# Kernel tuning notes

Measured on AMD Instinct MI355X. Metric: run time of the kernel, lower is better.

## Reference

```python
import jax, jax.numpy as jnp
import numpy as np

B, S, H = 2, 1024, 2048          # batch, seq, hidden
NH, HD = 32, 64                  # heads, head_dim
E, M, K = 8, 1024, 2             # experts, moe_dim, top_k
EPS = 1e-5
ROPE_THETA = 10000.0


def setup_inputs() -> dict:
    key = jax.random.key(0)
    ks = jax.random.split(key, 12)
    sc = lambda *sh: 0.02
    return {
        "hidden_states": jax.random.normal(ks[0], (B, S, H), jnp.float32),
        "w_attn_norm": jnp.ones((H,), jnp.float32),
        "Wq": jax.random.normal(ks[1], (H, H), jnp.float32) * 0.02,
        "Wk": jax.random.normal(ks[2], (H, H), jnp.float32) * 0.02,
        "Wv": jax.random.normal(ks[3], (H, H), jnp.float32) * 0.02,
        "Wo": jax.random.normal(ks[4], (H, H), jnp.float32) * 0.02,
        "w_moe_norm": jnp.ones((H,), jnp.float32),
        "Wr": jax.random.normal(ks[5], (H, E), jnp.float32) * 0.02,
        "Wgate": jax.random.normal(ks[6], (E, H, M), jnp.float32) * 0.02,
        "Wup": jax.random.normal(ks[7], (E, H, M), jnp.float32) * 0.02,
        "Wdown": jax.random.normal(ks[8], (E, M, H), jnp.float32) * 0.02,
    }


def _rmsnorm(x, w):
    return x * jax.lax.rsqrt(jnp.mean(x * x, axis=-1, keepdims=True) + EPS) * w


def _rope_cos_sin(seq_len, dtype):
    inv_freq = 1.0 / (ROPE_THETA ** (jnp.arange(0, HD, 2, dtype=jnp.float32) / HD))
    ang = jnp.arange(seq_len, dtype=jnp.float32)[:, None] * inv_freq[None, :]  # [S, HD/2]
    cos = jnp.concatenate([jnp.cos(ang), jnp.cos(ang)], axis=-1).astype(dtype)  # [S, HD]
    sin = jnp.concatenate([jnp.sin(ang), jnp.sin(ang)], axis=-1).astype(dtype)
    return cos, sin


def _rotate_half(x):
    x1, x2 = jnp.split(x, 2, axis=-1)
    return jnp.concatenate([-x2, x1], axis=-1)


def _attention(x, Wq, Wk, Wv, Wo, mask):
    b, s, _ = x.shape
    def heads(t):  # [b,s,H] -> [b,NH,s,HD]
        return t.reshape(b, s, NH, HD).transpose(0, 2, 1, 3)
    q, k, v = heads(x @ Wq), heads(x @ Wk), heads(x @ Wv)
    cos, sin = _rope_cos_sin(s, x.dtype)
    q = q * cos + _rotate_half(q) * sin
    k = k * cos + _rotate_half(k) * sin
    scores = jnp.einsum("bhqd,bhkd->bhqk", q, k) / jnp.sqrt(jnp.asarray(HD, x.dtype))
    scores = scores + mask  # [1,1,s,s] causal
    attn = jax.nn.softmax(scores, axis=-1)
    out = jnp.einsum("bhqk,bhkd->bhqd", attn, v)
    out = out.transpose(0, 2, 1, 3).reshape(b, s, H)
    return out @ Wo


def _moe(x, Wr, Wgate, Wup, Wdown):
    b, s, _ = x.shape
    xf = x.reshape(b * s, H)  # [T, H]
    logits = xf @ Wr  # [T, E]
    probs = jax.nn.softmax(logits, axis=-1)
    topv, topi = jax.lax.top_k(probs, K)  # [T, K]
    topv = topv / jnp.sum(topv, axis=-1, keepdims=True)
    # combine weights [T, E], zero for unselected experts
    cw = jnp.sum(jax.nn.one_hot(topi, E, dtype=xf.dtype) * topv[..., None], axis=1)
    g = jnp.einsum("th,ehm->etm", xf, Wgate)
    u = jnp.einsum("th,ehm->etm", xf, Wup)
    h = jax.nn.silu(g) * u
    expert_out = jnp.einsum("etm,emh->eth", h, Wdown)  # [E, T, H]
    out = jnp.einsum("eth,te->th", expert_out, cw)
    return out.reshape(b, s, H)


def reference(hidden_states, w_attn_norm, Wq, Wk, Wv, Wo, w_moe_norm, Wr, Wgate, Wup, Wdown):
    b, s, _ = hidden_states.shape
    causal = jnp.triu(jnp.full((s, s), -jnp.inf, hidden_states.dtype), k=1)[None, None]
    residual = hidden_states
    x = _rmsnorm(hidden_states, w_attn_norm)
    x = _attention(x, Wq, Wk, Wv, Wo, causal)
    x = x + residual
    residual = x
    y = _rmsnorm(x, w_moe_norm)
    y = _moe(y, Wr, Wgate, Wup, Wdown)
    return y + residual
```

## Files before the change

kernel.cpp:

```cpp
#include <hip/hip_runtime.h>
#include <hip/hip_bf16.h>
#include <cstdint>

typedef unsigned short u16;
typedef __bf16 bf16x4_t __attribute__((ext_vector_type(4)));
typedef __bf16 bf16x8_t __attribute__((ext_vector_type(8)));
typedef float f32x4_t __attribute__((ext_vector_type(4)));
typedef unsigned short us4_t __attribute__((ext_vector_type(4)));
typedef unsigned short us8_t __attribute__((ext_vector_type(8)));

#define BATCH 2
#define SEQ 1024
#define HID 2048
#define NHEAD 32
#define NEXP 8
#define MDIM 1024
#define T_TOK (BATCH*SEQ)


__device__ __forceinline__ void gload16(const void* g, void* l){
  __builtin_amdgcn_global_load_lds((__attribute__((address_space(1))) void*)(uintptr_t)g,
                                   (__attribute__((address_space(3))) void*)l, 16, 0, 0);
}

__device__ __forceinline__ bf16x8_t ldfrag(const u16* lo){
  bf16x4_t a = *(const bf16x4_t*)lo;
  bf16x4_t b = *(const bf16x4_t*)(lo + 16);
  return __builtin_shufflevector(a, b, 0,1,2,3,4,5,6,7);
}

__device__ __forceinline__ bf16x8_t ldfsw128(const u16* base, int row, int colbyte){
  const char* p = (const char*)base + row*128;
  int sw = (row & 7) << 4;
  bf16x4_t a = *(const bf16x4_t*)(p + (colbyte ^ sw));
  bf16x4_t b = *(const bf16x4_t*)(p + ((colbyte + 32) ^ sw));
  return __builtin_shufflevector(a, b, 0,1,2,3,4,5,6,7);
}

__device__ __forceinline__ bf16x8_t ldfsw64(const u16* base, int row, int colbyte){
  const char* p = (const char*)base + row*64;
  int sw = (row & 3) << 4;
  bf16x4_t a = *(const bf16x4_t*)(p + (colbyte ^ sw));
  bf16x4_t b = *(const bf16x4_t*)(p + ((colbyte + 32) ^ sw));
  return __builtin_shufflevector(a, b, 0,1,2,3,4,5,6,7);
}

__device__ __forceinline__ f32x4_t mfma16(bf16x8_t a, bf16x8_t b, f32x4_t c){
  return __builtin_amdgcn_mfma_f32_16x16x32_bf16(a, b, c, 0, 0, 0);
}

__device__ __forceinline__ u16 f2b(float f){
  __hip_bfloat16 h = __float2bfloat16(f);
  return __builtin_bit_cast(u16, h);
}
__device__ __forceinline__ float b2f(u16 b){
  return __builtin_bit_cast(float, (unsigned int)b << 16);
}
__device__ __forceinline__ void split3v(float v, u16& b1, u16& b2, u16& b3){
  b1 = f2b(v); float f1 = b2f(b1);
  float r1 = v - f1;
  b2 = f2b(r1); float f2 = b2f(b2);
  b3 = f2b(r1 - f2);
}



__global__ __launch_bounds__(256)
void convT(const float* __restrict__ in, u16* __restrict__ out, int R, int C)
{
  __shared__ float t[64][65];
  int bz = blockIdx.z;
  const float* ip = in + (size_t)bz * R * C;
  u16* op = out + (size_t)bz * R * C;
  int r0 = blockIdx.y*64, c0 = blockIdx.x*64;
  int tid = threadIdx.x;
  int lr = tid >> 4;
  int lc = (tid & 15) * 4;
  #pragma unroll
  for (int i = 0; i < 4; i++){
    int r = lr + i*16;
    float4 v = *(const float4*)&ip[(size_t)(r0 + r) * C + c0 + lc];
    t[r][lc] = v.x; t[r][lc+1] = v.y; t[r][lc+2] = v.z; t[r][lc+3] = v.w;
  }
  __syncthreads();
  #pragma unroll
  for (int i = 0; i < 4; i++){
    int c = lr + i*16;
    us4_t o;
    o.x = f2b(t[lc+0][c]); o.y = f2b(t[lc+1][c]);
    o.z = f2b(t[lc+2][c]); o.w = f2b(t[lc+3][c]);
    *(us4_t*)&op[(size_t)(c0 + c) * R + r0 + lc] = o;
  }
}


__global__ __launch_bounds__(256)
void convT3(const float* __restrict__ in, u16* __restrict__ o1, u16* __restrict__ o2,
            u16* __restrict__ o3)
{
  __shared__ float t[64][65];
  int r0 = blockIdx.y*64, c0 = blockIdx.x*64;
  int tid = threadIdx.x;
  int lr = tid >> 4;
  int lc = (tid & 15) * 4;
  #pragma unroll
  for (int i = 0; i < 4; i++){
    int r = lr + i*16;
    float4 v = *(const float4*)&in[(size_t)(r0 + r) * HID + c0 + lc];
    t[r][lc] = v.x; t[r][lc+1] = v.y; t[r][lc+2] = v.z; t[r][lc+3] = v.w;
  }
  __syncthreads();
  if (tid < 128){
    int n  = tid & 63;
    int kb2 = tid >> 6;
    int gn = c0 + n;
    int nb = gn >> 7, sub = (gn >> 4) & 7, fr = gn & 15;
    int kb = (r0 >> 5) + kb2;
    size_t fo = (((size_t)(nb*64 + kb)*8 + sub)*64 + fr*4) * 8;
    #pragma unroll
    for (int fg = 0; fg < 4; fg++){
      us8_t w1, w2, w3;
      #pragma unroll
      for (int j = 0; j < 4; j++){
        u16 b1, b2, b3;
        split3v(t[kb2*32 + fg*4 + j][n], b1, b2, b3);
        w1[j] = b1; w2[j] = b2; w3[j] = b3;
        split3v(t[kb2*32 + fg*4 + 16 + j][n], b1, b2, b3);
        w1[j+4] = b1; w2[j+4] = b2; w3[j+4] = b3;
      }
      *(us8_t*)&o1[fo + fg*8] = w1;
      *(us8_t*)&o2[fo + fg*8] = w2;
      *(us8_t*)&o3[fo + fg*8] = w3;
    }
  }
}


__global__ __launch_bounds__(256)
void rmsnorm3_k(const float* __restrict__ x, const float* __restrict__ w,
                u16* __restrict__ o1, u16* __restrict__ o2, u16* __restrict__ o3)
{
  int row = blockIdx.x;
  const float* xr = x + (size_t)row * HID;
  int tid = threadIdx.x;
  int kb = tid >> 2, fg = tid & 3;
  int kbase = kb*32 + fg*4;
  float4 a = *(const float4*)(xr + kbase);
  float4 b = *(const float4*)(xr + kbase + 16);
  float ss = a.x*a.x + a.y*a.y + a.z*a.z + a.w*a.w
           + b.x*b.x + b.y*b.y + b.z*b.z + b.w*b.w;
  #pragma unroll
  for (int off = 32; off; off >>= 1) ss += __shfl_down(ss, off);
  __shared__ float red[4];
  if ((tid & 63) == 0) red[tid >> 6] = ss;
  __syncthreads();
  float tot = red[0] + red[1] + red[2] + red[3];
  float rs = (float)(1.0 / sqrt((double)tot * (1.0/2048.0) + 1e-5));
  float4 wa = *(const float4*)(w + kbase);
  float4 wb = *(const float4*)(w + kbase + 16);
  float o[8];
  o[0]=a.x*rs*wa.x; o[1]=a.y*rs*wa.y; o[2]=a.z*rs*wa.z; o[3]=a.w*rs*wa.w;
  o[4]=b.x*rs*wb.x; o[5]=b.y*rs*wb.y; o[6]=b.z*rs*wb.z; o[7]=b.w*rs*wb.w;
  us8_t w1, w2, w3;
  #pragma unroll
  for (int j = 0; j < 8; j++){
    u16 b1, b2, b3; split3v(o[j], b1, b2, b3);
    w1[j] = b1; w2[j] = b2; w3[j] = b3;
  }
  int rb = row >> 7, sub = (row >> 4) & 7, fr = row & 15;
  size_t fo = (((size_t)(rb*64 + kb)*8 + sub)*64 + fr*4 + fg) * 8;
  *(us8_t*)&o1[fo] = w1; *(us8_t*)&o2[fo] = w2; *(us8_t*)&o3[fo] = w3;
}


__global__ __launch_bounds__(256)
void rmsnorm_k(const float* __restrict__ x, const float* __restrict__ w,
               u16* __restrict__ ob, float* __restrict__ of, float* __restrict__ oi)
{
  int row = blockIdx.x;
  const float* xr = x + (size_t)row * HID;
  int base = threadIdx.x * 8;
  float4 a = *(const float4*)(xr + base);
  float4 b = *(const float4*)(xr + base + 4);
  float ss = a.x*a.x + a.y*a.y + a.z*a.z + a.w*a.w
           + b.x*b.x + b.y*b.y + b.z*b.z + b.w*b.w;
  #pragma unroll
  for (int off = 32; off; off >>= 1) ss += __shfl_down(ss, off);
  __shared__ float red[4];
  if ((threadIdx.x & 63) == 0) red[threadIdx.x >> 6] = ss;
  __syncthreads();
  float tot = red[0] + red[1] + red[2] + red[3];
  float rs = (float)(1.0 / sqrt((double)tot * (1.0/2048.0) + 1e-5));
  float4 wa = *(const float4*)(w + base);
  float4 wb = *(const float4*)(w + base + 4);
  float o[8];
  o[0]=a.x*rs*wa.x; o[1]=a.y*rs*wa.y; o[2]=a.z*rs*wa.z; o[3]=a.w*rs*wa.w;
  o[4]=b.x*rs*wb.x; o[5]=b.y*rs*wb.y; o[6]=b.z*rs*wb.z; o[7]=b.w*rs*wb.w;
  us4_t p0, p1;
  p0.x=f2b(o[0]); p0.y=f2b(o[1]); p0.z=f2b(o[2]); p0.w=f2b(o[3]);
  p1.x=f2b(o[4]); p1.y=f2b(o[5]); p1.z=f2b(o[6]); p1.w=f2b(o[7]);
  *(us4_t*)&ob[(size_t)row*HID + base] = p0;
  *(us4_t*)&ob[(size_t)row*HID + base + 4] = p1;
  float* orow = of + (size_t)row*HID + base;
  *(float4*)orow = make_float4(o[0],o[1],o[2],o[3]);
  *(float4*)(orow+4) = make_float4(o[4],o[5],o[6],o[7]);
  float* irow = oi + (size_t)row*HID + base;
  *(float4*)irow = a;
  *(float4*)(irow+4) = b;
}


__global__ void rope_table_k(float* ct, float* st){
  int i = blockIdx.x*256 + threadIdx.x;
  int s = i >> 5, j = i & 31;
  double invf = exp(-(double)j / 32.0 * log(10000.0));
  double ang = (double)s * invf;
  ct[i] = (float)cos(ang);
  st[i] = (float)sin(ang);
}


__global__ __launch_bounds__(256, 2)
void gemm_qkv(const u16* __restrict__ A1, const u16* __restrict__ A2, const u16* __restrict__ A3,
              const u16* __restrict__ Wq1, const u16* __restrict__ Wq2, const u16* __restrict__ Wq3,
              const u16* __restrict__ Wk1, const u16* __restrict__ Wk2, const u16* __restrict__ Wk3,
              const u16* __restrict__ Wv1, const u16* __restrict__ Wv2, const u16* __restrict__ Wv3,
              u16* __restrict__ oq1, u16* __restrict__ oq2, u16* __restrict__ oq3,
              u16* __restrict__ ok1, u16* __restrict__ ok2, u16* __restrict__ ok3,
              float* __restrict__ vf,
              const float* __restrict__ ct, const float* __restrict__ st)
{
  __shared__ u16 As[3][128*32];
  __shared__ u16 Bs[3][128*32];
  const int flat = blockIdx.x + 16*blockIdx.y + 256*blockIdx.z;
  const int logical = (flat & 7) * 96 + (flat >> 3);
  const int z  = logical >> 8;
  const int bm = ((logical >> 4) & 15) * 128;
  const int bn = (logical & 15) * 128;
  const int tid = threadIdx.x;
  const int lane = tid & 63;
  const int wave = tid >> 6;
  const int wr = wave >> 1, wc = wave & 1;
  const int fr = lane & 15, fg = lane >> 4;

  f32x4_t acc[4][4] = {};

  const u16* Ap[3] = {A1, A2, A3};
  const u16* Bp[3];
  if (z == 0)      { Bp[0] = Wq1; Bp[1] = Wq2; Bp[2] = Wq3; }
  else if (z == 1) { Bp[0] = Wk1; Bp[1] = Wk2; Bp[2] = Wk3; }
  else             { Bp[0] = Wv1; Bp[1] = Wv2; Bp[2] = Wv3; }
  const u16* gA[3]; const u16* gB[3];
  #pragma unroll
  for (int t = 0; t < 3; t++){
    gA[t] = Ap[t] + (size_t)(bm >> 7) * 64 * 4096 + tid*8;
    gB[t] = Bp[t] + (size_t)(bn >> 7) * 64 * 4096 + tid*8;
  }

  for (int kb = 0; kb < 64; kb++){
    const size_t o = (size_t)kb * 4096;
    #pragma unroll
    for (int t = 0; t < 3; t++){
      gload16(gA[t] + o,        &As[t][tid*8]);
      gload16(gA[t] + o + 2048, &As[t][2048 + tid*8]);
      gload16(gB[t] + o,        &Bs[t][tid*8]);
      gload16(gB[t] + o + 2048, &Bs[t][2048 + tid*8]);
    }
    __syncthreads();
    bf16x8_t bfv[3][4];
    #pragma unroll
    for (int t = 0; t < 3; t++)
      #pragma unroll
      for (int ni = 0; ni < 4; ni++)
        bfv[t][ni] = *(const bf16x8_t*)&Bs[t][(((wc*4 + ni)*64) + fr*4 + fg)*8];
    #pragma unroll
    for (int mi = 0; mi < 4; mi++){
      const int ao = (((wr*4 + mi)*64) + fr*4 + fg)*8;
      bf16x8_t a1 = *(const bf16x8_t*)&As[0][ao];
      bf16x8_t a2 = *(const bf16x8_t*)&As[1][ao];
      bf16x8_t a3 = *(const bf16x8_t*)&As[2][ao];
      #pragma unroll
      for (int ni = 0; ni < 4; ni++){
        f32x4_t c = acc[mi][ni];
        c = mfma16(a3, bfv[0][ni], c);
        c = mfma16(a2, bfv[1][ni], c);
        c = mfma16(a1, bfv[2][ni], c);
        c = mfma16(a2, bfv[0][ni], c);
        c = mfma16(a1, bfv[1][ni], c);
        c = mfma16(a1, bfv[0][ni], c);
        acc[mi][ni] = c;
      }
    }
    __syncthreads();
  }

  if (z < 2){
    u16* O1 = z ? ok1 : oq1;
    u16* O2 = z ? ok2 : oq2;
    u16* O3 = z ? ok3 : oq3;
    #pragma unroll
    for (int mi = 0; mi < 4; mi++)
      #pragma unroll
      for (int r = 0; r < 4; r++){
        int row = bm + wr*64 + mi*16 + fg*4 + r;
        int s = row & (SEQ-1);
        #pragma unroll
        for (int ni = 0; ni < 2; ni++){
          int dlo = ni*16 + fr;
          float c  = ct[s*32 + dlo];
          float sn = st[s*32 + dlo];
          float xl = acc[mi][ni][r], xh = acc[mi][ni+2][r];
          float ol = xl*c - xh*sn;
          float oh = xh*c + xl*sn;
          size_t idx = (size_t)row * HID + bn + wc*64 + ni*16 + fr;
          u16 b1, b2, b3;
          split3v(ol, b1, b2, b3); O1[idx] = b1;    O2[idx] = b2;    O3[idx] = b3;
          split3v(oh, b1, b2, b3); O1[idx+32] = b1; O2[idx+32] = b2; O3[idx+32] = b3;
        }
      }
  } else {
    #pragma unroll
    for (int mi = 0; mi < 4; mi++)
      #pragma unroll
      for (int ni = 0; ni < 4; ni++)
        #pragma unroll
        for (int r = 0; r < 4; r++){
          int row = bm + wr*64 + mi*16 + fg*4 + r;
          int col = bn + wc*64 + ni*16 + fr;
          vf[(size_t)row * HID + col] = acc[mi][ni][r];
        }
  }
}


__global__ __launch_bounds__(256, 2)
void gemm_o(const u16* __restrict__ A1, const u16* __restrict__ A2, const u16* __restrict__ A3,
            const u16* __restrict__ B1, const u16* __restrict__ B2, const u16* __restrict__ B3,
            float* __restrict__ Cf, const float* __restrict__ Res)
{
  __shared__ u16 As[3][128*32];
  __shared__ u16 Bs[3][64*32];
  const int flat = blockIdx.x + 32*blockIdx.y;
  const int logical = (flat & 7) * 64 + (flat >> 3);
  const int bn = (logical & 31) * 64;
  const int bm = (logical >> 5) * 128;
  const int tid = threadIdx.x;
  const int lane = tid & 63;
  const int wave = tid >> 6;
  const int wr = wave >> 1, wc = wave & 1;
  const int fr = lane & 15, fg = lane >> 4;

  f32x4_t acc[4][2] = {};

  const u16* Ap[3] = {A1, A2, A3};
  const u16* Bp[3] = {B1, B2, B3};
  const u16* gA[3]; const u16* gB[3];
  const int sb0 = (bn >> 4) & 7;
  #pragma unroll
  for (int t = 0; t < 3; t++){
    gA[t] = Ap[t] + (size_t)(bm >> 7) * 64 * 4096 + tid*8;
    gB[t] = Bp[t] + (size_t)(bn >> 7) * 64 * 4096 + sb0*512 + tid*8;
  }

  for (int kb = 0; kb < 64; kb++){
    const size_t o = (size_t)kb * 4096;
    #pragma unroll
    for (int t = 0; t < 3; t++){
      gload16(gA[t] + o,        &As[t][tid*8]);
      gload16(gA[t] + o + 2048, &As[t][2048 + tid*8]);
      gload16(gB[t] + o,        &Bs[t][tid*8]);
    }
    __syncthreads();
    bf16x8_t bfv[3][2];
    #pragma unroll
    for (int t = 0; t < 3; t++)
      #pragma unroll
      for (int nj = 0; nj < 2; nj++)
        bfv[t][nj] = *(const bf16x8_t*)&Bs[t][(((wc*2 + nj)*64) + fr*4 + fg)*8];
    #pragma unroll
    for (int mi = 0; mi < 4; mi++){
      const int ao = (((wr*4 + mi)*64) + fr*4 + fg)*8;
      bf16x8_t a1 = *(const bf16x8_t*)&As[0][ao];
      bf16x8_t a2 = *(const bf16x8_t*)&As[1][ao];
      bf16x8_t a3 = *(const bf16x8_t*)&As[2][ao];
      #pragma unroll
      for (int nj = 0; nj < 2; nj++){
        f32x4_t c = acc[mi][nj];
        c = mfma16(a3, bfv[0][nj], c);
        c = mfma16(a2, bfv[1][nj], c);
        c = mfma16(a1, bfv[2][nj], c);
        c = mfma16(a2, bfv[0][nj], c);
        c = mfma16(a1, bfv[1][nj], c);
        c = mfma16(a1, bfv[0][nj], c);
        acc[mi][nj] = c;
      }
    }
    __syncthreads();
  }

  #pragma unroll
  for (int mi = 0; mi < 4; mi++)
    #pragma unroll
    for (int nj = 0; nj < 2; nj++)
      #pragma unroll
      for (int r = 0; r < 4; r++){
        int row = bm + wr*64 + mi*16 + fg*4 + r;
        int col = bn + wc*32 + nj*16 + fr;
        size_t idx = (size_t)row * HID + col;
        Cf[idx] = acc[mi][nj][r] + Res[idx];
      }
}


__global__ __launch_bounds__(256)
void split3_k(const float* __restrict__ in, u16* __restrict__ o1, u16* __restrict__ o2,
              u16* __restrict__ o3)
{
  int row = blockIdx.x;
  int tid = threadIdx.x;
  int kb = tid >> 2, fg = tid & 3;
  int kbase = kb*32 + fg*4;
  const float* xr = in + (size_t)row * HID;
  float4 a = *(const float4*)(xr + kbase);
  float4 b = *(const float4*)(xr + kbase + 16);
  float o[8] = {a.x, a.y, a.z, a.w, b.x, b.y, b.z, b.w};
  us8_t w1, w2, w3;
  #pragma unroll
  for (int j = 0; j < 8; j++){
    u16 b1, b2, b3; split3v(o[j], b1, b2, b3);
    w1[j] = b1; w2[j] = b2; w3[j] = b3;
  }
  int rb = row >> 7, sub = (row >> 4) & 7, fr = row & 15;
  size_t fo = (((size_t)(rb*64 + kb)*8 + sub)*64 + fr*4 + fg) * 8;
  *(us8_t*)&o1[fo] = w1; *(us8_t*)&o2[fo] = w2; *(us8_t*)&o3[fo] = w3;
}


__global__ __launch_bounds__(256)
void vtrans3_k(const float* __restrict__ vf, u16* __restrict__ t1, u16* __restrict__ t2,
               u16* __restrict__ t3)
{
  __shared__ float t[64][65];
  int st0 = blockIdx.x * 64;
  int bh = blockIdx.y;
  int b = bh >> 5, h = bh & 31;
  int tid = threadIdx.x;
  #pragma unroll
  for (int i = 0; i < 4; i++){
    int idx = tid + i*256;
    int s = idx >> 4, dc = (idx & 15) * 4;
    float4 v = *(const float4*)&vf[(size_t)(b*SEQ + st0 + s) * HID + h*64 + dc];
    t[dc+0][s] = v.x; t[dc+1][s] = v.y; t[dc+2][s] = v.z; t[dc+3][s] = v.w;
  }
  __syncthreads();
  #pragma unroll
  for (int i = 0; i < 4; i++){
    int idx = tid + i*256;
    int d = idx >> 4, sc = (idx & 15) * 4;
    us4_t v1, v2, v3;
    #pragma unroll
    for (int j = 0; j < 4; j++){
      u16 b1, b2, b3; split3v(t[d][sc+j], b1, b2, b3);
      v1[j]=b1; v2[j]=b2; v3[j]=b3;
    }
    size_t base = ((size_t)bh*64 + d)*SEQ + st0 + sc;
    *(us4_t*)&t1[base] = v1; *(us4_t*)&t2[base] = v2; *(us4_t*)&t3[base] = v3;
  }
}


__global__ __launch_bounds__(256)
void fattn3_k(const u16* __restrict__ q1, const u16* __restrict__ q2, const u16* __restrict__ q3,
              const u16* __restrict__ k1, const u16* __restrict__ k2, const u16* __restrict__ k3,
              const u16* __restrict__ v1, const u16* __restrict__ v2, const u16* __restrict__ v3,
              float* __restrict__ aof)
{
  __shared__ u16 Ks[3][64*64];
  __shared__ u16 Vs[3][64*64];
  __shared__ u16 Ps[2][4][16*64];
  const int bh = blockIdx.x, qt = blockIdx.y;
  const int b = bh >> 5, h = bh & 31;
  const int tid = threadIdx.x, lane = tid & 63, wave = tid >> 6;
  const int fr = lane & 15, fg = lane >> 4;

  const size_t qrow = (size_t)(b*SEQ + qt*64 + wave*16 + fr);
  const u16* qp[3] = { q1 + qrow*HID + h*64, q2 + qrow*HID + h*64, q3 + qrow*HID + h*64 };
  bf16x8_t aq[3][2];
  #pragma unroll
  for (int t = 0; t < 3; t++)
    #pragma unroll
    for (int ks = 0; ks < 2; ks++) aq[t][ks] = ldfrag(qp[t] + ks*32 + fg*4);

  f32x4_t oacc[4] = {};
  float m_r[4], l_r[4];
  #pragma unroll
  for (int r = 0; r < 4; r++){ m_r[r] = -1e30f; l_r[r] = 0.f; }

  const int sr = tid >> 3, sp = (tid & 7) ^ (sr & 7);
  const u16* kb[3] = { k1 + ((size_t)(b*SEQ) + sr)*HID + h*64 + sp*8,
                       k2 + ((size_t)(b*SEQ) + sr)*HID + h*64 + sp*8,
                       k3 + ((size_t)(b*SEQ) + sr)*HID + h*64 + sp*8 };
  const u16* vb[3] = { v1 + ((size_t)bh*64 + sr)*SEQ + sp*8,
                       v2 + ((size_t)bh*64 + sr)*SEQ + sp*8,
                       v3 + ((size_t)bh*64 + sr)*SEQ + sp*8 };

  for (int kt = 0; kt <= qt; kt++){
    #pragma unroll
    for (int t = 0; t < 3; t++){
      gload16(kb[t] + (size_t)(kt*64) * HID,    &Ks[t][tid*8]);
      gload16(kb[t] + (size_t)(kt*64+32) * HID, &Ks[t][2048 + tid*8]);
      gload16(vb[t] + kt*64,                    &Vs[t][tid*8]);
      gload16(vb[t] + (size_t)32*SEQ + kt*64,   &Vs[t][2048 + tid*8]);
    }
    __syncthreads();

    f32x4_t sc[4] = {};
    #pragma unroll
    for (int nf = 0; nf < 4; nf++)
      #pragma unroll
      for (int ks = 0; ks < 2; ks++){
        int krow = nf*16 + fr, kcb = ks*64 + fg*8;
        bf16x8_t bk0 = ldfsw128(Ks[0], krow, kcb);
        bf16x8_t bk1 = ldfsw128(Ks[1], krow, kcb);
        bf16x8_t bk2 = ldfsw128(Ks[2], krow, kcb);
        sc[nf] = mfma16(aq[2][ks], bk0, sc[nf]);
        sc[nf] = mfma16(aq[1][ks], bk1, sc[nf]);
        sc[nf] = mfma16(aq[0][ks], bk2, sc[nf]);
        sc[nf] = mfma16(aq[1][ks], bk0, sc[nf]);
        sc[nf] = mfma16(aq[0][ks], bk1, sc[nf]);
        sc[nf] = mfma16(aq[0][ks], bk0, sc[nf]);
      }

    float nm[4] = {-1e30f,-1e30f,-1e30f,-1e30f};
    #pragma unroll
    for (int nf = 0; nf < 4; nf++)
      #pragma unroll
      for (int r = 0; r < 4; r++){
        float v = sc[nf][r] * 0.125f;
        if (kt == qt && nf*16 + fr > wave*16 + fg*4 + r) v = -1e30f;
        sc[nf][r] = v;
        nm[r] = fmaxf(nm[r], v);
      }
    #pragma unroll
    for (int r = 0; r < 4; r++)
      #pragma unroll
      for (int msk = 8; msk; msk >>= 1) nm[r] = fmaxf(nm[r], __shfl_xor(nm[r], msk));

    #pragma unroll
    for (int r = 0; r < 4; r++){
      float mn = fmaxf(m_r[r], nm[r]);
      float f = __expf(m_r[r] - mn);
      m_r[r] = mn;
      float rsum = 0.f;
      #pragma unroll
      for (int nf = 0; nf < 4; nf++){
        float pv = __expf(sc[nf][r] - mn);
        sc[nf][r] = pv;
        rsum += pv;
      }
      #pragma unroll
      for (int msk = 8; msk; msk >>= 1) rsum += __shfl_xor(rsum, msk);
      l_r[r] = l_r[r]*f + rsum;
      #pragma unroll
      for (int df = 0; df < 4; df++) oacc[df][r] *= f;
    }

    #pragma unroll
    for (int nf = 0; nf < 4; nf++)
      #pragma unroll
      for (int r = 0; r < 4; r++){
        float pv = sc[nf][r];
        u16 b1 = f2b(pv);
        float f1 = b2f(b1);
        u16 b2 = f2b(pv - f1);
        int prow = fg*4 + r;
        int pbyte = (nf*32 + fr*2) ^ ((prow & 7) << 4);
        *(u16*)((char*)&Ps[0][wave][0] + prow*128 + pbyte) = b1;
        *(u16*)((char*)&Ps[1][wave][0] + prow*128 + pbyte) = b2;
      }

    #pragma unroll
    for (int ks = 0; ks < 2; ks++){
      bf16x8_t pa0 = ldfsw128(&Ps[0][wave][0], fr, ks*64 + fg*8);
      bf16x8_t pa1 = ldfsw128(&Ps[1][wave][0], fr, ks*64 + fg*8);
      #pragma unroll
      for (int df = 0; df < 4; df++){
        int vrow = df*16 + fr, vcb = ks*64 + fg*8;
        bf16x8_t bv0 = ldfsw128(Vs[0], vrow, vcb);
        bf16x8_t bv1 = ldfsw128(Vs[1], vrow, vcb);
        bf16x8_t bv2 = ldfsw128(Vs[2], vrow, vcb);
        oacc[df] = mfma16(pa0, bv2, oacc[df]);
        oacc[df] = mfma16(pa1, bv1, oacc[df]);
        oacc[df] = mfma16(pa1, bv0, oacc[df]);
        oacc[df] = mfma16(pa0, bv1, oacc[df]);
        oacc[df] = mfma16(pa0, bv0, oacc[df]);
      }
    }
    __syncthreads();
  }

  #pragma unroll
  for (int r = 0; r < 4; r++){
    float inv = 1.f / l_r[r];
    int orow = b*SEQ + qt*64 + wave*16 + fg*4 + r;
    #pragma unroll
    for (int df = 0; df < 4; df++)
      aof[(size_t)orow * HID + h*64 + df*16 + fr] = oacc[df][r] * inv;
  }
}


__global__ __launch_bounds__(64)
void router_scatter_k(const float* __restrict__ yn, const float* __restrict__ Wr,
                      int* __restrict__ tok_list, float* __restrict__ w_list,
                      int* __restrict__ cur){
  int row = blockIdx.x;
  int lane = threadIdx.x;
  const float* xr = yn + (size_t)row * HID;
  double acc[8] = {};
  for (int j = lane; j < HID; j += 64){
    double xv = (double)xr[j];
    const float* wr = Wr + (size_t)j*8;
    float4 w0 = *(const float4*)wr;
    float4 w1 = *(const float4*)(wr + 4);
    acc[0] += xv*w0.x; acc[1] += xv*w0.y; acc[2] += xv*w0.z; acc[3] += xv*w0.w;
    acc[4] += xv*w1.x; acc[5] += xv*w1.y; acc[6] += xv*w1.z; acc[7] += xv*w1.w;
  }
  #pragma unroll
  for (int e = 0; e < 8; e++)
    #pragma unroll
    for (int off = 32; off; off >>= 1) acc[e] += __shfl_down(acc[e], off);
  if (lane == 0){
    double mx = acc[0];
    #pragma unroll
    for (int e = 1; e < 8; e++) mx = fmax(mx, acc[e]);
    double p[8];
    #pragma unroll
    for (int e = 0; e < 8; e++) p[e] = exp(acc[e] - mx);
    int i1 = 0;
    #pragma unroll
    for (int e = 1; e < 8; e++) if (p[e] > p[i1]) i1 = e;
    int i2 = (i1 == 0) ? 1 : 0;
    #pragma unroll
    for (int e = 0; e < 8; e++) if (e != i1 && p[e] > p[i2]) i2 = e;
    double s2 = p[i1] + p[i2];
    int pos1 = atomicAdd(&cur[i1], 1);
    tok_list[i1*T_TOK + pos1] = row;
    w_list[i1*T_TOK + pos1] = (float)(p[i1] / s2);
    int pos2 = atomicAdd(&cur[i2], 1);
    tok_list[i2*T_TOK + pos2] = row;
    w_list[i2*T_TOK + pos2] = (float)(p[i2] / s2);
  }
}

__global__ __launch_bounds__(128)
void pad_k(const int* __restrict__ cur, int* __restrict__ tok_list,
           float* __restrict__ w_list, int* __restrict__ cnt_pad){
  int e = blockIdx.x;
  int c = cur[e];
  int cp = (c + 127) & ~127;
  for (int i = c + threadIdx.x; i < cp; i += 128){
    tok_list[e*T_TOK + i] = 0;
    w_list[e*T_TOK + i] = 0.f;
  }
  if (threadIdx.x == 0) cnt_pad[e] = cp;
}


__global__ __launch_bounds__(256, 2)
void gemm_gateup_sp(const u16* __restrict__ A, const u16* __restrict__ WgT, const u16* __restrict__ WuT,
                    const int* __restrict__ tok_list, const float* __restrict__ w_list,
                    const int* __restrict__ cnt_pad, u16* __restrict__ Hb)
{
  const int e = blockIdx.z;
  const int bm = blockIdx.y * 128;
  if (bm >= cnt_pad[e]) return;
  __shared__ u16 As[128*32];
  __shared__ u16 Bg[64*32];
  __shared__ u16 Bu[64*32];
  const int tid = threadIdx.x;
  const int lane = tid & 63;
  const int wave = tid >> 6;
  const int wr = wave >> 1, wc = wave & 1;
  const int fr = lane & 15, fg = lane >> 4;
  const int bn = blockIdx.x * 64;

  f32x4_t ag[4][2] = {}, au[4][2] = {};

  const int srow = tid >> 2, skb = (tid & 3) ^ (srow & 3);
  const int tok0 = tok_list[e*T_TOK + bm + srow];
  const int tok1 = tok_list[e*T_TOK + bm + srow + 64];
  const u16* ga0 = A + (size_t)tok0 * HID + skb * 8;
  const u16* ga1 = A + (size_t)tok1 * HID + skb * 8;
  const u16* gg0 = WgT + ((size_t)e*MDIM + bn + srow) * HID + skb * 8;
  const u16* gu0 = WuT + ((size_t)e*MDIM + bn + srow) * HID + skb * 8;

  for (int kk = 0; kk < HID; kk += 32){
    gload16(ga0 + kk, &As[tid*8]);
    gload16(ga1 + kk, &As[2048 + tid*8]);
    gload16(gg0 + kk, &Bg[tid*8]);
    gload16(gu0 + kk, &Bu[tid*8]);
    __syncthreads();
    bf16x8_t af[4], bg[2], bu[2];
    #pragma unroll
    for (int i = 0; i < 4; i++) af[i] = ldfsw64(As, wr*64 + i*16 + fr, fg*8);
    #pragma unroll
    for (int j = 0; j < 2; j++){
      bg[j] = ldfsw64(Bg, wc*32 + j*16 + fr, fg*8);
      bu[j] = ldfsw64(Bu, wc*32 + j*16 + fr, fg*8);
    }
    #pragma unroll
    for (int mi = 0; mi < 4; mi++)
      #pragma unroll
      for (int nj = 0; nj < 2; nj++){
        ag[mi][nj] = mfma16(af[mi], bg[nj], ag[mi][nj]);
        au[mi][nj] = mfma16(af[mi], bu[nj], au[mi][nj]);
      }
    __syncthreads();
  }

  #pragma unroll
  for (int mi = 0; mi < 4; mi++)
    #pragma unroll
    for (int nj = 0; nj < 2; nj++)
      #pragma unroll
      for (int r = 0; r < 4; r++){
        int pos = bm + wr*64 + mi*16 + fg*4 + r;
        int col = bn + wc*32 + nj*16 + fr;
        float g = ag[mi][nj][r], u = au[mi][nj][r];
        float h = g / (1.0f + __expf(-g)) * u * w_list[e*T_TOK + pos];
        Hb[((size_t)e*T_TOK + pos)*MDIM + col] = f2b(h);
      }
}


__global__ __launch_bounds__(256, 2)
void gemm_down_sp(const u16* __restrict__ Hb, const u16* __restrict__ WdT,
                  const int* __restrict__ tok_list, const int* __restrict__ cnt_pad,
                  float* __restrict__ Out)
{
  const int e = blockIdx.z;
  const int bm = blockIdx.y * 128;
  if (bm >= cnt_pad[e]) return;
  __shared__ u16 As[128*32];
  __shared__ u16 Bs[128*32];
  const int tid = threadIdx.x;
  const int lane = tid & 63;
  const int wave = tid >> 6;
  const int wr = wave >> 1, wc = wave & 1;
  const int fr = lane & 15, fg = lane >> 4;
  const int bn = blockIdx.x * 128;
  const int srow = tid >> 2, skb = (tid & 3) ^ (srow & 3);

  f32x4_t acc[4][4] = {};

  const u16* A  = Hb  + (size_t)e * T_TOK * MDIM;
  const u16* Bt = WdT + (size_t)e * HID * MDIM;
  const u16* ga0 = A + (size_t)(bm + srow) * MDIM + skb * 8;
  const u16* gb0 = Bt + (size_t)(bn + srow) * MDIM + skb * 8;
  for (int kk = 0; kk < MDIM; kk += 32){
    gload16(ga0 + kk, &As[tid*8]);
    gload16(ga0 + (size_t)64*MDIM + kk, &As[2048 + tid*8]);
    gload16(gb0 + kk, &Bs[tid*8]);
    gload16(gb0 + (size_t)64*MDIM + kk, &Bs[2048 + tid*8]);
    __syncthreads();
    bf16x8_t af[4], bfv[4];
    #pragma unroll
    for (int i = 0; i < 4; i++) af[i]  = ldfsw64(As, wr*64 + i*16 + fr, fg*8);
    #pragma unroll
    for (int i = 0; i < 4; i++) bfv[i] = ldfsw64(Bs, wc*64 + i*16 + fr, fg*8);
    #pragma unroll
    for (int mi = 0; mi < 4; mi++)
      #pragma unroll
      for (int ni = 0; ni < 4; ni++)
        acc[mi][ni] = mfma16(af[mi], bfv[ni], acc[mi][ni]);
    __syncthreads();
  }

  #pragma unroll
  for (int mi = 0; mi < 4; mi++)
    #pragma unroll
    for (int r = 0; r < 4; r++){
      int pos = bm + wr*64 + mi*16 + fg*4 + r;
      int tok = tok_list[e*T_TOK + pos];
      #pragma unroll
      for (int ni = 0; ni < 4; ni++){
        int col = bn + wc*64 + ni*16 + fr;
        atomicAdd(&Out[(size_t)tok * HID + col], acc[mi][ni][r]);
      }
    }
}


extern "C" void kernel_launch(void* const* d_in, const int* in_sizes, int n_in,
                              void* d_out, int out_size, void* d_ws, size_t ws_size,
                              hipStream_t stream)
{
  const float* hs     = (const float*)d_in[0];
  const float* w_attn = (const float*)d_in[1];
  const float* Wq = (const float*)d_in[2];
  const float* Wk = (const float*)d_in[3];
  const float* Wv = (const float*)d_in[4];
  const float* Wo = (const float*)d_in[5];
  const float* w_moe = (const float*)d_in[6];
  const float* Wr = (const float*)d_in[7];
  const float* Wg = (const float*)d_in[8];
  const float* Wu = (const float*)d_in[9];
  const float* Wd = (const float*)d_in[10];
  float* out = (float*)d_out;
  (void)in_sizes; (void)n_in; (void)out_size; (void)ws_size;

  char* ws = (char*)d_ws;
  const size_t MB = 1024*1024;
  char* R0 = ws;
  char* R1 = ws + 96*MB;
  char* R2 = ws + 120*MB;
  char* R3 = ws + 144*MB;
  char* R4 = ws + 168*MB;
  char* RS = ws + 184*MB;

  const size_t WSLB = (size_t)HID*HID;
  u16* W0 = (u16*)R0;
  u16 *Wq1 = W0,          *Wq2 = W0 + WSLB,    *Wq3 = W0 + 2*WSLB;
  u16 *Wk1 = W0 + 3*WSLB, *Wk2 = W0 + 4*WSLB,  *Wk3 = W0 + 5*WSLB;
  u16 *Wv1 = W0 + 6*WSLB, *Wv2 = W0 + 7*WSLB,  *Wv3 = W0 + 8*WSLB;
  u16 *Wo1 = W0 + 9*WSLB, *Wo2 = W0 + 10*WSLB, *Wo3 = W0 + 11*WSLB;
  const size_t TSLB = (size_t)T_TOK*HID;
  u16 *xn1 = (u16*)R1, *xn2 = (u16*)R1 + TSLB, *xn3 = (u16*)R1 + 2*TSLB;
  u16 *q1  = (u16*)R2, *q2  = (u16*)R2 + TSLB, *q3  = (u16*)R2 + 2*TSLB;
  u16 *k1  = (u16*)R3, *k2  = (u16*)R3 + TSLB, *k3  = (u16*)R3 + 2*TSLB;
  u16 *vt1 = xn1, *vt2 = xn2, *vt3 = xn3;
  float* vf  = (float*)R4;
  float* aof = (float*)R4;
  u16 *ao1 = k1, *ao2 = k2, *ao3 = k3;
  float* x1  = (float*)R4;
  u16* WgT = (u16*)R0;
  u16* WuT = (u16*)R0 + (size_t)NEXP*MDIM*HID;
  u16* WdT = (u16*)R0 + 2*(size_t)NEXP*MDIM*HID;
  u16* ynb = (u16*)R1;
  float* yn = (float*)(R1 + 8*MB);
  u16* hb  = (u16*)R2;
  int*   tok_list = (int*)RS;
  float* w_list   = (float*)(RS + 64*1024);
  int*   cur      = (int*)(RS + 128*1024);
  int*   cnt_pad  = (int*)(RS + 132*1024);
  float* ct   = (float*)(RS + 256*1024);
  float* stab = (float*)(RS + 384*1024);

  dim3 blk256(256), gMoE(16,16,8);

  rope_table_k<<<dim3(SEQ*32/256), blk256, 0, stream>>>(ct, stab);
  convT3<<<dim3(HID/64, HID/64), blk256, 0, stream>>>(Wq, Wq1, Wq2, Wq3);
  convT3<<<dim3(HID/64, HID/64), blk256, 0, stream>>>(Wk, Wk1, Wk2, Wk3);
  convT3<<<dim3(HID/64, HID/64), blk256, 0, stream>>>(Wv, Wv1, Wv2, Wv3);
  convT3<<<dim3(HID/64, HID/64), blk256, 0, stream>>>(Wo, Wo1, Wo2, Wo3);

  rmsnorm3_k<<<dim3(T_TOK), blk256, 0, stream>>>(hs, w_attn, xn1, xn2, xn3);

  gemm_qkv<<<dim3(16,16,3), blk256, 0, stream>>>(xn1,xn2,xn3,
      Wq1,Wq2,Wq3, Wk1,Wk2,Wk3, Wv1,Wv2,Wv3,
      q1,q2,q3, k1,k2,k3, vf, ct, stab);

  vtrans3_k<<<dim3(SEQ/64, BATCH*NHEAD), blk256, 0, stream>>>(vf, vt1, vt2, vt3);

  fattn3_k<<<dim3(BATCH*NHEAD, SEQ/64), blk256, 0, stream>>>(q1,q2,q3, k1,k2,k3, vt1,vt2,vt3, aof);

  split3_k<<<dim3(T_TOK), blk256, 0, stream>>>(aof, ao1, ao2, ao3);

  gemm_o<<<dim3(32,16), blk256, 0, stream>>>(ao1,ao2,ao3, Wo1,Wo2,Wo3, x1, hs);

  convT<<<dim3(MDIM/64, HID/64, NEXP), blk256, 0, stream>>>(Wg, WgT, HID, MDIM);
  convT<<<dim3(MDIM/64, HID/64, NEXP), blk256, 0, stream>>>(Wu, WuT, HID, MDIM);
  convT<<<dim3(HID/64, MDIM/64, NEXP), blk256, 0, stream>>>(Wd, WdT, MDIM, HID);

  rmsnorm_k<<<dim3(T_TOK), blk256, 0, stream>>>(x1, w_moe, ynb, yn, out);

  hipMemsetAsync(cur, 0, NEXP*sizeof(int), stream);
  router_scatter_k<<<dim3(T_TOK), dim3(64), 0, stream>>>(yn, Wr, tok_list, w_list, cur);
  pad_k<<<dim3(NEXP), dim3(128), 0, stream>>>(cur, tok_list, w_list, cnt_pad);

  gemm_gateup_sp<<<gMoE, blk256, 0, stream>>>(ynb, WgT, WuT, tok_list, w_list, cnt_pad, hb);
  gemm_down_sp<<<gMoE, blk256, 0, stream>>>(hb, WdT, tok_list, cnt_pad, out);
}
```

Before: 922.1 us.

## Store Q/K/V, attention output and MoE weights in MFMA fragment-linear layouts

Q, K and transposed V are now written in a per-head fragment-ordered layout, so the attention kernel copies contiguous tiles and reads MFMA fragments with single 16-byte LDS loads instead of swizzled paired loads. The attention kernel now writes its output already split into three bf16 parts in the layout gemm_o expects, which removes the separate split3_k pass and its fp32 round trip. The MoE weight conversion writes fragment-linear tiles so the expert GEMMs load B operands contiguously. The cost is scattered 2-byte stores in the QKV and attention epilogues, and possible LDS bank conflicts from the unswizzled fragment reads.

```diff
diff --git a/kernel.cpp b/kernel.cpp
--- a/kernel.cpp
+++ b/kernel.cpp
@@ -23,20 +23,6 @@
                                    (__attribute__((address_space(3))) void*)l, 16, 0, 0);
 }
 
-__device__ __forceinline__ bf16x8_t ldfrag(const u16* lo){
-  bf16x4_t a = *(const bf16x4_t*)lo;
-  bf16x4_t b = *(const bf16x4_t*)(lo + 16);
-  return __builtin_shufflevector(a, b, 0,1,2,3,4,5,6,7);
-}
-
-__device__ __forceinline__ bf16x8_t ldfsw128(const u16* base, int row, int colbyte){
-  const char* p = (const char*)base + row*128;
-  int sw = (row & 7) << 4;
-  bf16x4_t a = *(const bf16x4_t*)(p + (colbyte ^ sw));
-  bf16x4_t b = *(const bf16x4_t*)(p + ((colbyte + 32) ^ sw));
-  return __builtin_shufflevector(a, b, 0,1,2,3,4,5,6,7);
-}
-
 __device__ __forceinline__ bf16x8_t ldfsw64(const u16* base, int row, int colbyte){
   const char* p = (const char*)base + row*64;
   int sw = (row & 3) << 4;
@@ -66,9 +52,10 @@
 
 
 __global__ __launch_bounds__(256)
-void convT(const float* __restrict__ in, u16* __restrict__ out, int R, int C)
+void convT_fl(const float* __restrict__ in, u16* __restrict__ out, int R, int C)
 {
   __shared__ float t[64][65];
+  const int KB = C >> 5;
   int bz = blockIdx.z;
   const float* ip = in + (size_t)bz * R * C;
   u16* op = out + (size_t)bz * R * C;
@@ -79,17 +66,27 @@
   #pragma unroll
   for (int i = 0; i < 4; i++){
     int r = lr + i*16;
-    float4 v = *(const float4*)&ip[(size_t)(r0 + r) * C + c0 + lc];
+    float4 v = *(const float4*)&ip[(size_t)(r0 + r) * R + c0 + lc];
     t[r][lc] = v.x; t[r][lc+1] = v.y; t[r][lc+2] = v.z; t[r][lc+3] = v.w;
   }
   __syncthreads();
-  #pragma unroll
-  for (int i = 0; i < 4; i++){
-    int c = lr + i*16;
-    us4_t o;
-    o.x = f2b(t[lc+0][c]); o.y = f2b(t[lc+1][c]);
-    o.z = f2b(t[lc+2][c]); o.w = f2b(t[lc+3][c]);
-    *(us4_t*)&op[(size_t)(c0 + c) * R + r0 + lc] = o;
+  if (tid < 128){
+    int n_l = tid & 63;
+    int kb2 = tid >> 6;
+    int gn = c0 + n_l;
+    int rb = gn >> 7, sub = (gn >> 4) & 7, frn = gn & 15;
+    int kb = (r0 >> 5) + kb2;
+    size_t fo = (((size_t)(rb*KB + kb)*8 + sub)*64 + frn*4) * 8;
+    #pragma unroll
+    for (int fg = 0; fg < 4; fg++){
+      us8_t w;
+      #pragma unroll
+      for (int j = 0; j < 4; j++){
+        w[j]   = f2b(t[kb2*32 + fg*4 + j][n_l]);
+        w[j+4] = f2b(t[kb2*32 + fg*4 + 16 + j][n_l]);
+      }
+      *(us8_t*)&op[fo + fg*8] = w;
+    }
   }
 }
 
@@ -298,12 +295,18 @@
     u16* O1 = z ? ok1 : oq1;
     u16* O2 = z ? ok2 : oq2;
     u16* O3 = z ? ok3 : oq3;
+    const int h = (bn + wc*64) >> 6;
     #pragma unroll
     for (int mi = 0; mi < 4; mi++)
       #pragma unroll
       for (int r = 0; r < 4; r++){
         int row = bm + wr*64 + mi*16 + fg*4 + r;
         int s = row & (SEQ-1);
+        int b = row >> 10;
+        int tok = row & 1023;
+        int tb = tok >> 4;
+        int frk = fg*4 + r;
+        size_t sb = (size_t)(b*NHEAD + h) * 65536;
         #pragma unroll
         for (int ni = 0; ni < 2; ni++){
           int dlo = ni*16 + fr;
@@ -312,10 +315,11 @@
           float xl = acc[mi][ni][r], xh = acc[mi][ni+2][r];
           float ol = xl*c - xh*sn;
           float oh = xh*c + xl*sn;
-          size_t idx = (size_t)row * HID + bn + wc*64 + ni*16 + fr;
+          size_t a0 = sb + ((size_t)(tb*2 + 0)*64 + frk*4 + (fr>>2))*8 + ni*4 + (fr&3);
+          size_t a1 = sb + ((size_t)(tb*2 + 1)*64 + frk*4 + (fr>>2))*8 + ni*4 + (fr&3);
           u16 b1, b2, b3;
-          split3v(ol, b1, b2, b3); O1[idx] = b1;    O2[idx] = b2;    O3[idx] = b3;
-          split3v(oh, b1, b2, b3); O1[idx+32] = b1; O2[idx+32] = b2; O3[idx+32] = b3;
+          split3v(ol, b1, b2, b3); O1[a0] = b1; O2[a0] = b2; O3[a0] = b3;
+          split3v(oh, b1, b2, b3); O1[a1] = b1; O2[a1] = b2; O3[a1] = b3;
         }
       }
   } else {
@@ -413,30 +417,6 @@
 
 
 __global__ __launch_bounds__(256)
-void split3_k(const float* __restrict__ in, u16* __restrict__ o1, u16* __restrict__ o2,
-              u16* __restrict__ o3)
-{
-  int row = blockIdx.x;
-  int tid = threadIdx.x;
-  int kb = tid >> 2, fg = tid & 3;
-  int kbase = kb*32 + fg*4;
-  const float* xr = in + (size_t)row * HID;
-  float4 a = *(const float4*)(xr + kbase);
-  float4 b = *(const float4*)(xr + kbase + 16);
-  float o[8] = {a.x, a.y, a.z, a.w, b.x, b.y, b.z, b.w};
-  us8_t w1, w2, w3;
-  #pragma unroll
-  for (int j = 0; j < 8; j++){
-    u16 b1, b2, b3; split3v(o[j], b1, b2, b3);
-    w1[j] = b1; w2[j] = b2; w3[j] = b3;
-  }
-  int rb = row >> 7, sub = (row >> 4) & 7, fr = row & 15;
-  size_t fo = (((size_t)(rb*64 + kb)*8 + sub)*64 + fr*4 + fg) * 8;
-  *(us8_t*)&o1[fo] = w1; *(us8_t*)&o2[fo] = w2; *(us8_t*)&o3[fo] = w3;
-}
-
-
-__global__ __launch_bounds__(256)
 void vtrans3_k(const float* __restrict__ vf, u16* __restrict__ t1, u16* __restrict__ t2,
                u16* __restrict__ t3)
 {
@@ -454,17 +434,23 @@
   }
   __syncthreads();
   #pragma unroll
-  for (int i = 0; i < 4; i++){
-    int idx = tid + i*256;
-    int d = idx >> 4, sc = (idx & 15) * 4;
-    us4_t v1, v2, v3;
-    #pragma unroll
-    for (int j = 0; j < 4; j++){
-      u16 b1, b2, b3; split3v(t[d][sc+j], b1, b2, b3);
-      v1[j]=b1; v2[j]=b2; v3[j]=b3;
-    }
-    size_t base = ((size_t)bh*64 + d)*SEQ + st0 + sc;
-    *(us4_t*)&t1[base] = v1; *(us4_t*)&t2[base] = v2; *(us4_t*)&t3[base] = v3;
+  for (int it = 0; it < 2; it++){
+    int rho = tid + it*256;
+    int kbv_l = rho >> 8;
+    int db    = (rho >> 6) & 3;
+    int lane  = rho & 63;
+    int d = db*16 + (lane >> 2);
+    int fgv = lane & 3;
+    us8_t w1, w2, w3;
+    #pragma unroll
+    for (int j = 0; j < 8; j++){
+      int half = j >> 2, e = j & 3;
+      int tokl = kbv_l*32 + half*16 + fgv*4 + e;
+      u16 b1, b2, b3; split3v(t[d][tokl], b1, b2, b3);
+      w1[j] = b1; w2[j] = b2; w3[j] = b3;
+    }
+    size_t base = (size_t)bh*65536 + ((size_t)(((st0>>5) + kbv_l)*4 + db)*64 + lane)*8;
+    *(us8_t*)&t1[base] = w1; *(us8_t*)&t2[base] = w2; *(us8_t*)&t3[base] = w3;
   }
 }
 
@@ -473,44 +459,41 @@
 void fattn3_k(const u16* __restrict__ q1, const u16* __restrict__ q2, const u16* __restrict__ q3,
               const u16* __restrict__ k1, const u16* __restrict__ k2, const u16* __restrict__ k3,
               const u16* __restrict__ v1, const u16* __restrict__ v2, const u16* __restrict__ v3,
-              float* __restrict__ aof)
-{
-  __shared__ u16 Ks[3][64*64];
-  __shared__ u16 Vs[3][64*64];
-  __shared__ u16 Ps[2][4][16*64];
+              u16* __restrict__ ao1, u16* __restrict__ ao2, u16* __restrict__ ao3)
+{
+  __shared__ u16 Ks[3][4096];
+  __shared__ u16 Vs[3][4096];
+  __shared__ u16 Ps[2][4][1024];
   const int bh = blockIdx.x, qt = blockIdx.y;
   const int b = bh >> 5, h = bh & 31;
   const int tid = threadIdx.x, lane = tid & 63, wave = tid >> 6;
   const int fr = lane & 15, fg = lane >> 4;
-
-  const size_t qrow = (size_t)(b*SEQ + qt*64 + wave*16 + fr);
-  const u16* qp[3] = { q1 + qrow*HID + h*64, q2 + qrow*HID + h*64, q3 + qrow*HID + h*64 };
+  const size_t hslab = (size_t)bh * 65536;
+
   bf16x8_t aq[3][2];
-  #pragma unroll
-  for (int t = 0; t < 3; t++)
-    #pragma unroll
-    for (int ks = 0; ks < 2; ks++) aq[t][ks] = ldfrag(qp[t] + ks*32 + fg*4);
+  {
+    size_t qo = hslab + (size_t)(qt*4 + wave)*1024 + (size_t)(fr*4 + fg)*8;
+    aq[0][0] = *(const bf16x8_t*)&q1[qo]; aq[0][1] = *(const bf16x8_t*)&q1[qo + 512];
+    aq[1][0] = *(const bf16x8_t*)&q2[qo]; aq[1][1] = *(const bf16x8_t*)&q2[qo + 512];
+    aq[2][0] = *(const bf16x8_t*)&q3[qo]; aq[2][1] = *(const bf16x8_t*)&q3[qo + 512];
+  }
 
   f32x4_t oacc[4] = {};
   float m_r[4], l_r[4];
   #pragma unroll
   for (int r = 0; r < 4; r++){ m_r[r] = -1e30f; l_r[r] = 0.f; }
 
-  const int sr = tid >> 3, sp = (tid & 7) ^ (sr & 7);
-  const u16* kb[3] = { k1 + ((size_t)(b*SEQ) + sr)*HID + h*64 + sp*8,
-                       k2 + ((size_t)(b*SEQ) + sr)*HID + h*64 + sp*8,
-                       k3 + ((size_t)(b*SEQ) + sr)*HID + h*64 + sp*8 };
-  const u16* vb[3] = { v1 + ((size_t)bh*64 + sr)*SEQ + sp*8,
-                       v2 + ((size_t)bh*64 + sr)*SEQ + sp*8,
-                       v3 + ((size_t)bh*64 + sr)*SEQ + sp*8 };
+  const u16* kp[3] = { k1 + hslab, k2 + hslab, k3 + hslab };
+  const u16* vp[3] = { v1 + hslab, v2 + hslab, v3 + hslab };
 
   for (int kt = 0; kt <= qt; kt++){
+    const size_t o = (size_t)kt * 4096;
     #pragma unroll
     for (int t = 0; t < 3; t++){
-      gload16(kb[t] + (size_t)(kt*64) * HID,    &Ks[t][tid*8]);
-      gload16(kb[t] + (size_t)(kt*64+32) * HID, &Ks[t][2048 + tid*8]);
-      gload16(vb[t] + kt*64,                    &Vs[t][tid*8]);
-      gload16(vb[t] + (size_t)32*SEQ + kt*64,   &Vs[t][2048 + tid*8]);
+      gload16(kp[t] + o + tid*8,        &Ks[t][tid*8]);
+      gload16(kp[t] + o + 2048 + tid*8, &Ks[t][2048 + tid*8]);
+      gload16(vp[t] + o + tid*8,        &Vs[t][tid*8]);
+      gload16(vp[t] + o + 2048 + tid*8, &Vs[t][2048 + tid*8]);
     }
     __syncthreads();
 
@@ -519,10 +502,10 @@
     for (int nf = 0; nf < 4; nf++)
       #pragma unroll
       for (int ks = 0; ks < 2; ks++){
-        int krow = nf*16 + fr, kcb = ks*64 + fg*8;
-        bf16x8_t bk0 = ldfsw128(Ks[0], krow, kcb);
-        bf16x8_t bk1 = ldfsw128(Ks[1], krow, kcb);
-        bf16x8_t bk2 = ldfsw128(Ks[2], krow, kcb);
+        const int ko = ((nf*2 + ks)*64 + fr*4 + fg)*8;
+        bf16x8_t bk0 = *(const bf16x8_t*)&Ks[0][ko];
+        bf16x8_t bk1 = *(const bf16x8_t*)&Ks[1][ko];
+        bf16x8_t bk2 = *(const bf16x8_t*)&Ks[2][ko];
         sc[nf] = mfma16(aq[2][ks], bk0, sc[nf]);
         sc[nf] = mfma16(aq[1][ks], bk1, sc[nf]);
         sc[nf] = mfma16(aq[0][ks], bk2, sc[nf]);
@@ -573,22 +556,21 @@
         u16 b1 = f2b(pv);
         float f1 = b2f(b1);
         u16 b2 = f2b(pv - f1);
-        int prow = fg*4 + r;
-        int pbyte = (nf*32 + fr*2) ^ ((prow & 7) << 4);
-        *(u16*)((char*)&Ps[0][wave][0] + prow*128 + pbyte) = b1;
-        *(u16*)((char*)&Ps[1][wave][0] + prow*128 + pbyte) = b2;
+        int pa = ((nf>>1)*64 + (fg*4 + r)*4 + (fr>>2))*8 + (nf&1)*4 + (fr&3);
+        Ps[0][wave][pa] = b1;
+        Ps[1][wave][pa] = b2;
       }
 
     #pragma unroll
     for (int ks = 0; ks < 2; ks++){
-      bf16x8_t pa0 = ldfsw128(&Ps[0][wave][0], fr, ks*64 + fg*8);
-      bf16x8_t pa1 = ldfsw128(&Ps[1][wave][0], fr, ks*64 + fg*8);
+      bf16x8_t pa0 = *(const bf16x8_t*)&Ps[0][wave][(ks*64 + fr*4 + fg)*8];
+      bf16x8_t pa1 = *(const bf16x8_t*)&Ps[1][wave][(ks*64 + fr*4 + fg)*8];
       #pragma unroll
       for (int df = 0; df < 4; df++){
-        int vrow = df*16 + fr, vcb = ks*64 + fg*8;
-        bf16x8_t bv0 = ldfsw128(Vs[0], vrow, vcb);
-        bf16x8_t bv1 = ldfsw128(Vs[1], vrow, vcb);
-        bf16x8_t bv2 = ldfsw128(Vs[2], vrow, vcb);
+        const int vo = ((ks*4 + df)*64 + fr*4 + fg)*8;
+        bf16x8_t bv0 = *(const bf16x8_t*)&Vs[0][vo];
+        bf16x8_t bv1 = *(const bf16x8_t*)&Vs[1][vo];
+        bf16x8_t bv2 = *(const bf16x8_t*)&Vs[2][vo];
         oacc[df] = mfma16(pa0, bv2, oacc[df]);
         oacc[df] = mfma16(pa1, bv1, oacc[df]);
         oacc[df] = mfma16(pa1, bv0, oacc[df]);
@@ -603,9 +585,15 @@
   for (int r = 0; r < 4; r++){
     float inv = 1.f / l_r[r];
     int orow = b*SEQ + qt*64 + wave*16 + fg*4 + r;
-    #pragma unroll
-    for (int df = 0; df < 4; df++)
-      aof[(size_t)orow * HID + h*64 + df*16 + fr] = oacc[df][r] * inv;
+    int rb = orow >> 7, sub = (orow >> 4) & 7, frA = orow & 15;
+    #pragma unroll
+    for (int df = 0; df < 4; df++){
+      float val = oacc[df][r] * inv;
+      int kb = h*2 + (df >> 1);
+      size_t addr = ((((size_t)rb*64 + kb)*8 + sub)*64 + frA*4 + (fr>>2))*8 + (df&1)*4 + (fr&3);
+      u16 b1, b2, b3; split3v(val, b1, b2, b3);
+      ao1[addr] = b1; ao2[addr] = b2; ao3[addr] = b3;
+    }
   }
 }
 
@@ -692,22 +680,23 @@
   const int tok1 = tok_list[e*T_TOK + bm + srow + 64];
   const u16* ga0 = A + (size_t)tok0 * HID + skb * 8;
   const u16* ga1 = A + (size_t)tok1 * HID + skb * 8;
-  const u16* gg0 = WgT + ((size_t)e*MDIM + bn + srow) * HID + skb * 8;
-  const u16* gu0 = WuT + ((size_t)e*MDIM + bn + srow) * HID + skb * 8;
-
-  for (int kk = 0; kk < HID; kk += 32){
-    gload16(ga0 + kk, &As[tid*8]);
-    gload16(ga1 + kk, &As[2048 + tid*8]);
-    gload16(gg0 + kk, &Bg[tid*8]);
-    gload16(gu0 + kk, &Bu[tid*8]);
+  const int sub0 = (bn >> 4) & 7;
+  const u16* gg = WgT + (size_t)e*MDIM*HID + ((size_t)(bn>>7)*512 + sub0)*512 + tid*8;
+  const u16* gu = WuT + (size_t)e*MDIM*HID + ((size_t)(bn>>7)*512 + sub0)*512 + tid*8;
+
+  for (int kb = 0; kb < 64; kb++){
+    gload16(ga0 + kb*32, &As[tid*8]);
+    gload16(ga1 + kb*32, &As[2048 + tid*8]);
+    gload16(gg + (size_t)kb*4096, &Bg[tid*8]);
+    gload16(gu + (size_t)kb*4096, &Bu[tid*8]);
     __syncthreads();
     bf16x8_t af[4], bg[2], bu[2];
     #pragma unroll
     for (int i = 0; i < 4; i++) af[i] = ldfsw64(As, wr*64 + i*16 + fr, fg*8);
     #pragma unroll
     for (int j = 0; j < 2; j++){
-      bg[j] = ldfsw64(Bg, wc*32 + j*16 + fr, fg*8);
-      bu[j] = ldfsw64(Bu, wc*32 + j*16 + fr, fg*8);
+      bg[j] = *(const bf16x8_t*)&Bg[((wc*2 + j)*64 + fr*4 + fg)*8];
+      bu[j] = *(const bf16x8_t*)&Bu[((wc*2 + j)*64 + fr*4 + fg)*8];
     }
     #pragma unroll
     for (int mi = 0; mi < 4; mi++)
@@ -755,20 +744,19 @@
   f32x4_t acc[4][4] = {};
 
   const u16* A  = Hb  + (size_t)e * T_TOK * MDIM;
-  const u16* Bt = WdT + (size_t)e * HID * MDIM;
   const u16* ga0 = A + (size_t)(bm + srow) * MDIM + skb * 8;
-  const u16* gb0 = Bt + (size_t)(bn + srow) * MDIM + skb * 8;
-  for (int kk = 0; kk < MDIM; kk += 32){
-    gload16(ga0 + kk, &As[tid*8]);
-    gload16(ga0 + (size_t)64*MDIM + kk, &As[2048 + tid*8]);
-    gload16(gb0 + kk, &Bs[tid*8]);
-    gload16(gb0 + (size_t)64*MDIM + kk, &Bs[2048 + tid*8]);
+  const u16* gB = WdT + (size_t)e*HID*MDIM + (size_t)(bn>>7)*131072 + tid*8;
+  for (int kb = 0; kb < 32; kb++){
+    gload16(ga0 + kb*32, &As[tid*8]);
+    gload16(ga0 + (size_t)64*MDIM + kb*32, &As[2048 + tid*8]);
+    gload16(gB + (size_t)kb*4096,        &Bs[tid*8]);
+    gload16(gB + (size_t)kb*4096 + 2048, &Bs[2048 + tid*8]);
     __syncthreads();
     bf16x8_t af[4], bfv[4];
     #pragma unroll
     for (int i = 0; i < 4; i++) af[i]  = ldfsw64(As, wr*64 + i*16 + fr, fg*8);
     #pragma unroll
-    for (int i = 0; i < 4; i++) bfv[i] = ldfsw64(Bs, wc*64 + i*16 + fr, fg*8);
+    for (int i = 0; i < 4; i++) bfv[i] = *(const bf16x8_t*)&Bs[((wc*4 + i)*64 + fr*4 + fg)*8];
     #pragma unroll
     for (int mi = 0; mi < 4; mi++)
       #pragma unroll
@@ -817,7 +805,8 @@
   char* R2 = ws + 120*MB;
   char* R3 = ws + 144*MB;
   char* R4 = ws + 168*MB;
-  char* RS = ws + 184*MB;
+  char* R5 = ws + 184*MB;
+  char* RS = ws + 208*MB;
 
   const size_t WSLB = (size_t)HID*HID;
   u16* W0 = (u16*)R0;
@@ -831,9 +820,8 @@
   u16 *k1  = (u16*)R3, *k2  = (u16*)R3 + TSLB, *k3  = (u16*)R3 + 2*TSLB;
   u16 *vt1 = xn1, *vt2 = xn2, *vt3 = xn3;
   float* vf  = (float*)R4;
-  float* aof = (float*)R4;
-  u16 *ao1 = k1, *ao2 = k2, *ao3 = k3;
   float* x1  = (float*)R4;
+  u16 *ao1 = (u16*)R5, *ao2 = (u16*)R5 + TSLB, *ao3 = (u16*)R5 + 2*TSLB;
   u16* WgT = (u16*)R0;
   u16* WuT = (u16*)R0 + (size_t)NEXP*MDIM*HID;
   u16* WdT = (u16*)R0 + 2*(size_t)NEXP*MDIM*HID;
@@ -863,15 +851,14 @@
 
   vtrans3_k<<<dim3(SEQ/64, BATCH*NHEAD), blk256, 0, stream>>>(vf, vt1, vt2, vt3);
 
-  fattn3_k<<<dim3(BATCH*NHEAD, SEQ/64), blk256, 0, stream>>>(q1,q2,q3, k1,k2,k3, vt1,vt2,vt3, aof);
-
-  split3_k<<<dim3(T_TOK), blk256, 0, stream>>>(aof, ao1, ao2, ao3);
+  fattn3_k<<<dim3(BATCH*NHEAD, SEQ/64), blk256, 0, stream>>>(q1,q2,q3, k1,k2,k3,
+      vt1,vt2,vt3, ao1,ao2,ao3);
 
   gemm_o<<<dim3(32,16), blk256, 0, stream>>>(ao1,ao2,ao3, Wo1,Wo2,Wo3, x1, hs);
 
-  convT<<<dim3(MDIM/64, HID/64, NEXP), blk256, 0, stream>>>(Wg, WgT, HID, MDIM);
-  convT<<<dim3(MDIM/64, HID/64, NEXP), blk256, 0, stream>>>(Wu, WuT, HID, MDIM);
-  convT<<<dim3(HID/64, MDIM/64, NEXP), blk256, 0, stream>>>(Wd, WdT, MDIM, HID);
+  convT_fl<<<dim3(MDIM/64, HID/64, NEXP), blk256, 0, stream>>>(Wg, WgT, MDIM, HID);
+  convT_fl<<<dim3(MDIM/64, HID/64, NEXP), blk256, 0, stream>>>(Wu, WuT, MDIM, HID);
+  convT_fl<<<dim3(HID/64, MDIM/64, NEXP), blk256, 0, stream>>>(Wd, WdT, HID, MDIM);
 
   rmsnorm_k<<<dim3(T_TOK), blk256, 0, stream>>>(x1, w_moe, ynb, yn, out);
 
```

New measurement: 843.8 us. 8.5% less time.
